# Kernel tuning notes

Hardware: AMD Instinct MI355X
Metric: run time of the kernel (lower is better)

## Reference

```python
import jax, jax.numpy as jnp
import numpy as np

B, S, D, H, DM = 2, 2048, 1024, 16, 4
HD = D // H  # head_dim = 64
EPS = 1e-5


def setup_inputs() -> dict:
    key = jax.random.key(0)
    ks = jax.random.split(key, 8)
    s = 0.02
    return {
        "x": jax.random.normal(ks[0], (B, S, D), jnp.float32),
        "wq": jax.random.normal(ks[1], (D, D), jnp.float32) * s,
        "wk": jax.random.normal(ks[2], (D, D), jnp.float32) * s,
        "wv": jax.random.normal(ks[3], (D, D), jnp.float32) * s,
        "wo": jax.random.normal(ks[4], (D, D), jnp.float32) * s,
        "bo": jnp.zeros((D,), jnp.float32),
        "ln1_scale": jnp.ones((D,), jnp.float32),
        "ln1_shift": jnp.zeros((D,), jnp.float32),
        "ln2_scale": jnp.ones((D,), jnp.float32),
        "ln2_shift": jnp.zeros((D,), jnp.float32),
        "w1": jax.random.normal(ks[5], (DM * D, D), jnp.float32) * s,
        "b1": jnp.zeros((DM * D,), jnp.float32),
        "w2": jax.random.normal(ks[6], (D, DM * D), jnp.float32) * s,
        "b2": jnp.zeros((D,), jnp.float32),
    }


def _layernorm(x, scale, shift):
    mean = jnp.mean(x, axis=-1, keepdims=True)
    var = jnp.var(x, axis=-1, keepdims=True)  # unbiased=False
    return scale * (x - mean) * jax.lax.rsqrt(var + EPS) + shift


def _attn(x, wq, wk, wv, wo, bo):
    b, n, d = x.shape
    # torch Linear: y = x @ W.T
    q = (x @ wq.T).reshape(b, n, H, HD).transpose(0, 2, 1, 3)  # [b,h,n,hd]
    k = (x @ wk.T).reshape(b, n, H, HD).transpose(0, 2, 1, 3)
    v = (x @ wv.T).reshape(b, n, H, HD).transpose(0, 2, 1, 3)
    scores = jnp.einsum("bhqd,bhkd->bhqk", q, k)
    causal = jnp.tril(jnp.ones((n, n), bool))
    scores = jnp.where(causal, scores, -jnp.inf)
    w = jax.nn.softmax(scores / np.sqrt(HD).astype(np.float32), axis=-1)
    ctx = jnp.einsum("bhqk,bhkd->bhqd", w, v)
    ctx = ctx.transpose(0, 2, 1, 3).reshape(b, n, d)
    return ctx @ wo.T + bo


def reference(x, wq, wk, wv, wo, bo, ln1_scale, ln1_shift, ln2_scale, ln2_shift, w1, b1, w2, b2):
    h = x + _attn(_layernorm(x, ln1_scale, ln1_shift), wq, wk, wv, wo, bo)
    y = _layernorm(h, ln2_scale, ln2_shift)
    y = jax.nn.relu(y @ w1.T + b1) @ w2.T + b2
    return h + y
```

## Files before the change

kernel.cpp:

```cpp
#include <hip/hip_runtime.h>
#include <hip/hip_bf16.h>

#define DEV __device__ __forceinline__

typedef __attribute__((ext_vector_type(8))) short bf8;
typedef __attribute__((ext_vector_type(4))) float f4;
typedef __attribute__((ext_vector_type(16))) float f16x;

DEV unsigned short f2bf(float f) {
  union { __hip_bfloat16 h; unsigned short u; } c;
  c.h = __float2bfloat16(f);
  return c.u;
}
DEV unsigned int pk2(float a, float b) {
  union { __hip_bfloat162 h; unsigned int u; } c;
  c.h = __hip_bfloat162(__float2bfloat16(a), __float2bfloat16(b));
  return c.u;
}

DEV int2 swz_tile(int ob, int nxt, int nyt) {
  const int nb = nxt * nyt;
  const int cpx = nb >> 3;
  const int W = (ob & 7) * cpx + (ob >> 3);
  const int scw = 4 * nyt;
  const int sc = W / scw, rem = W - sc * scw;
  return make_int2(rem >> 2, sc * 4 + (rem & 3));
}

template<bool BIAS, bool RELU, bool OUTBF, bool WRVT>
__global__ __launch_bounds__(512, 2) void gemm_bt256(
    const unsigned short* __restrict__ A, const unsigned short* __restrict__ B,
    const float* __restrict__ bias, void* __restrict__ Cout,
    int M, int N, int K, int ldc, unsigned short* __restrict__ vtout, int nyt)
{
  __shared__ unsigned short Sl[2][2][256 * 64];
  const int t = threadIdx.x;
  const int w = t >> 6, l = t & 63;
  const int wr = w >> 2, wc = w & 3;
  int2 tt = swz_tile((int)blockIdx.x, N >> 8, nyt);
  const int m0 = tt.x * 256, n0 = tt.y * 256;

  const int srow = w * 32 + (l >> 3);
  const int scol = 8 * ((l & 7) ^ (l >> 3));
  const unsigned short* Ab = A + (size_t)(m0 + srow) * K + scol;
  const unsigned short* Bb = B + (size_t)(n0 + srow) * K + scol;
  const int sdst = w * 2048 + l * 8;

  auto STAGE = [&](int slot, int kt) {
#pragma unroll
    for (int i = 0; i < 4; ++i) {
      __builtin_amdgcn_global_load_lds(
          (const __attribute__((address_space(1))) void*)(Ab + (size_t)i * 8 * K + kt * 64),
          (__attribute__((address_space(3))) void*)(&Sl[slot][0][sdst + i * 512]), 16, 0, 0);
      __builtin_amdgcn_global_load_lds(
          (const __attribute__((address_space(1))) void*)(Bb + (size_t)i * 8 * K + kt * 64),
          (__attribute__((address_space(3))) void*)(&Sl[slot][1][sdst + i * 512]), 16, 0, 0);
    }
  };

  const f4 fz = {0.f, 0.f, 0.f, 0.f};
  f4 acc[8][4];
#pragma unroll
  for (int i = 0; i < 8; ++i)
#pragma unroll
    for (int j = 0; j < 4; ++j) acc[i][j] = fz;

  const int NT = K >> 6;
  STAGE(0, 0);
  __syncthreads();

  for (int T = 0; T < NT; ++T) {
    if (T + 1 < NT) STAGE((T + 1) & 1, T + 1);
    const int sl = T & 1;
#pragma unroll
    for (int ks = 0; ks < 2; ++ks) {
      const int cb = (ks * 64 + ((l >> 4) * 16)) ^ ((l & 7) << 4);
      bf8 af[8], bg[4];
#pragma unroll
      for (int m = 0; m < 8; ++m)
        af[m] = *(const bf8*)((const char*)&Sl[sl][0][(wr * 128 + m * 16 + (l & 15)) * 64] + cb);
#pragma unroll
      for (int n = 0; n < 4; ++n)
        bg[n] = *(const bf8*)((const char*)&Sl[sl][1][(wc * 64 + n * 16 + (l & 15)) * 64] + cb);
      __builtin_amdgcn_s_setprio(1);
#pragma unroll
      for (int m = 0; m < 8; ++m)
#pragma unroll
        for (int n = 0; n < 4; ++n)
          acc[m][n] = __builtin_amdgcn_mfma_f32_16x16x32_bf16(af[m], bg[n], acc[m][n], 0, 0, 0);
      __builtin_amdgcn_s_setprio(0);
    }
    __syncthreads();
  }

#pragma unroll
  for (int n = 0; n < 4; ++n) {
    const int col = n0 + wc * 64 + n * 16 + (l & 15);
    float bv = 0.f;
    if (BIAS) bv = bias[col];
    const bool isv = WRVT && (col >= 2048);
    const int hh = (col - 2048) >> 6, dd = (col - 2048) & 63;
#pragma unroll
    for (int m = 0; m < 8; ++m) {
#pragma unroll
      for (int r = 0; r < 4; ++r) {
        const int row = m0 + wr * 128 + m * 16 + ((l >> 4) * 4) + r;
        float v = acc[m][n][r] + bv;
        if (RELU) v = fmaxf(v, 0.f);
        if (WRVT && isv) {
          const int bb = row >> 11, ss = row & 2047;
          vtout[((size_t)(bb * 16 + hh) * 64 + dd) * 2048 + ss] = f2bf(v);
        } else if (OUTBF) {
          ((unsigned short*)Cout)[(size_t)row * ldc + col] = f2bf(v);
        } else {
          ((float*)Cout)[(size_t)row * ldc + col] = v;
        }
      }
    }
  }
}

template<bool BIAS, bool RELU, bool RESID, bool OUTBF>
__global__ __launch_bounds__(256) void gemm_bt(
    const unsigned short* __restrict__ A, const unsigned short* __restrict__ B,
    const float* __restrict__ bias, const float* __restrict__ resid,
    void* __restrict__ Cout, int M, int N, int K, int ldc, int nyt)
{
  __shared__ unsigned short Al[2][128 * 32];
  __shared__ unsigned short Bl[2][128 * 32];
  const int t = threadIdx.x;
  const int w = t >> 6, l = t & 63;
  const int wr = w >> 1, wc = w & 1;
  int2 tt = swz_tile((int)blockIdx.x, N >> 7, nyt);
  const int m0 = tt.x * 128, n0 = tt.y * 128;

  const int srow = w * 16 + (l >> 2);
  const int scsw = ((l & 3) * 8) ^ (((srow >> 1) & 3) << 3);
  const unsigned short* Ab = A + (size_t)(m0 + srow) * K + scsw;
  const unsigned short* Bb = B + (size_t)(n0 + srow) * K + scsw;
  const int sdst = w * 512 + l * 8;

  auto STAGE = [&](int slot, int k0) {
#pragma unroll
    for (int i = 0; i < 2; ++i) {
      __builtin_amdgcn_global_load_lds(
          (const __attribute__((address_space(1))) void*)(Ab + (size_t)i * 64 * K + k0),
          (__attribute__((address_space(3))) void*)(&Al[slot][sdst + i * 2048]), 16, 0, 0);
      __builtin_amdgcn_global_load_lds(
          (const __attribute__((address_space(1))) void*)(Bb + (size_t)i * 64 * K + k0),
          (__attribute__((address_space(3))) void*)(&Bl[slot][sdst + i * 2048]), 16, 0, 0);
    }
  };

  const f4 fz = {0.f, 0.f, 0.f, 0.f};
  f4 acc[4][4];
#pragma unroll
  for (int i = 0; i < 4; ++i)
#pragma unroll
    for (int j = 0; j < 4; ++j) acc[i][j] = fz;

  const int NT = K >> 5;
  STAGE(0, 0);
  __syncthreads();

  for (int T = 0; T < NT; ++T) {
    if (T + 1 < NT) STAGE((T + 1) & 1, (T + 1) * 32);
    const int sl = T & 1;
    const int rdcol = ((l >> 4) * 8) ^ ((((l & 15) >> 1) & 3) << 3);
    bf8 af[4], bg[4];
#pragma unroll
    for (int am = 0; am < 4; ++am)
      af[am] = *(const bf8*)&Al[sl][(wr * 64 + am * 16 + (l & 15)) * 32 + rdcol];
#pragma unroll
    for (int bn = 0; bn < 4; ++bn)
      bg[bn] = *(const bf8*)&Bl[sl][(wc * 64 + bn * 16 + (l & 15)) * 32 + rdcol];
    __builtin_amdgcn_s_setprio(1);
#pragma unroll
    for (int am = 0; am < 4; ++am)
#pragma unroll
      for (int bn = 0; bn < 4; ++bn)
        acc[am][bn] = __builtin_amdgcn_mfma_f32_16x16x32_bf16(af[am], bg[bn], acc[am][bn], 0, 0, 0);
    __builtin_amdgcn_s_setprio(0);
    __syncthreads();
  }

#pragma unroll
  for (int bn = 0; bn < 4; ++bn) {
    const int col = n0 + wc * 64 + bn * 16 + (l & 15);
    float bv = 0.f;
    if (BIAS) bv = bias[col];
#pragma unroll
    for (int am = 0; am < 4; ++am) {
#pragma unroll
      for (int r = 0; r < 4; ++r) {
        const int row = m0 + wr * 64 + am * 16 + ((l >> 4) * 4) + r;
        float v = acc[am][bn][r] + bv;
        if (RELU) v = fmaxf(v, 0.f);
        if (RESID) v += resid[(size_t)row * ldc + col];
        if (OUTBF) ((unsigned short*)Cout)[(size_t)row * ldc + col] = f2bf(v);
        else       ((float*)Cout)[(size_t)row * ldc + col] = v;
      }
    }
  }
}

__global__ __launch_bounds__(128, 2) void attn_kernel(
    const unsigned short* __restrict__ qk, const unsigned short* __restrict__ vt,
    unsigned short* __restrict__ ctx)
{
  __shared__ unsigned short Ks[2][64 * 64];
  __shared__ unsigned short Vs[2][64 * 64];

  const int t = threadIdx.x;
  const int w = t >> 6, l = t & 63;
  const int hi = l >> 5, q = l & 31;
  const int j = blockIdx.x;
  const int h = blockIdx.y, b = blockIdx.z;
  const unsigned short* qbase = qk + ((size_t)b * 2048) * 2048 + h * 64;
  const unsigned short* kbase = qbase + 1024;
  const unsigned short* vbase = vt + ((size_t)(b * 16 + h)) * 64 * 2048;

  auto STAGE = [&](int buf, int it) {
#pragma unroll
    for (int s = 0; s < 4; ++s) {
      const int row = s * 16 + (t >> 3);
      const int cb = (t & 7) * 16;
      const int sb = cb ^ ((row & 7) << 4);
      __builtin_amdgcn_global_load_lds(
          (const __attribute__((address_space(1))) void*)
              (kbase + (size_t)(it * 64 + row) * 2048 + (sb >> 1)),
          (__attribute__((address_space(3))) void*)(&Ks[buf][row * 64 + (cb >> 1)]),
          16, 0, 0);
      __builtin_amdgcn_global_load_lds(
          (const __attribute__((address_space(1))) void*)
              (vbase + (size_t)row * 2048 + it * 64 + (sb >> 1)),
          (__attribute__((address_space(3))) void*)(&Vs[buf][row * 64 + (cb >> 1)]),
          16, 0, 0);
    }
  };

  for (int pass = 0; pass < 2; ++pass) {
    const int qtile = pass ? j : 31 - j;
    const int q0w = qtile * 64 + w * 32;
    bf8 qf[4];
#pragma unroll
    for (int ksl = 0; ksl < 4; ++ksl)
      qf[ksl] = *(const bf8*)(qbase + (size_t)(q0w + q) * 2048 + ksl * 16 + hi * 8);

    f16x oacc[2];
#pragma unroll
    for (int dn = 0; dn < 2; ++dn)
#pragma unroll
      for (int i = 0; i < 16; ++i) oacc[dn][i] = 0.f;
    float m_ = -1e30f, l_ = 0.f;

    const int nit = qtile + 1;
    STAGE(0, 0);
    __syncthreads();

    for (int it = 0; it < nit; ++it) {
      const int buf = it & 1;
      if (it + 1 < nit) STAGE(buf ^ 1, it + 1);
      const int kb0 = it * 64;

      f16x s0, s1;
#pragma unroll
      for (int i = 0; i < 16; ++i) { s0[i] = 0.f; s1[i] = 0.f; }
#pragma unroll
      for (int ksl = 0; ksl < 4; ++ksl) {
        const int cbq = ((ksl * 16 + hi * 8) * 2);
        const int r0 = q, r1 = 32 + q;
        bf8 k0 = *(const bf8*)((const char*)&Ks[buf][r0 * 64] + (cbq ^ ((r0 & 7) << 4)));
        bf8 k1 = *(const bf8*)((const char*)&Ks[buf][r1 * 64] + (cbq ^ ((r1 & 7) << 4)));
        s0 = __builtin_amdgcn_mfma_f32_32x32x16_bf16(k0, qf[ksl], s0, 0, 0, 0);
        s1 = __builtin_amdgcn_mfma_f32_32x32x16_bf16(k1, qf[ksl], s1, 0, 0, 0);
      }

      float p[32];
      if (kb0 + 63 > q0w) {
#pragma unroll
        for (int i = 0; i < 16; ++i) {
          const int key = kb0 + (i & 3) + 8 * (i >> 2) + 4 * hi;
          p[i]      = (key <= q0w + q)      ? s0[i] : -1e30f;
          p[16 + i] = (key + 32 <= q0w + q) ? s1[i] : -1e30f;
        }
      } else {
#pragma unroll
        for (int i = 0; i < 16; ++i) { p[i] = s0[i]; p[16 + i] = s1[i]; }
      }

      float tm[16];
#pragma unroll
      for (int i = 0; i < 16; ++i) tm[i] = fmaxf(p[i], p[16 + i]);
#pragma unroll
      for (int st = 8; st >= 1; st >>= 1)
#pragma unroll
        for (int i = 0; i < 8; ++i)
          if (i < st) tm[i] = fmaxf(tm[i], tm[i + st]);
      const float pmax = fmaxf(tm[0], __shfl_xor(tm[0], 32));
      if (__any(pmax > m_ + 8.0f)) {
        const float mn = fmaxf(m_, pmax);
        const float alpha = __expf(m_ - mn);
        m_ = mn;
        l_ *= alpha;
#pragma unroll
        for (int dn = 0; dn < 2; ++dn)
#pragma unroll
          for (int i = 0; i < 16; ++i) oacc[dn][i] *= alpha;
      }
#pragma unroll
      for (int i = 0; i < 32; ++i) p[i] = __expf(p[i] - m_);
      float ts[16];
#pragma unroll
      for (int i = 0; i < 16; ++i) ts[i] = p[i] + p[16 + i];
#pragma unroll
      for (int st = 8; st >= 1; st >>= 1)
#pragma unroll
        for (int i = 0; i < 8; ++i)
          if (i < st) ts[i] += ts[i + st];
      l_ += ts[0] + __shfl_xor(ts[0], 32);

#pragma unroll
      for (int sg = 0; sg < 2; ++sg) {
        const float* pp = p + sg * 16;
        unsigned int wds[8];
#pragma unroll
        for (int m = 0; m < 4; ++m) {
          wds[m * 2]     = pk2(pp[4 * m], pp[4 * m + 1]);
          wds[m * 2 + 1] = pk2(pp[4 * m + 2], pp[4 * m + 3]);
        }
#pragma unroll
        for (int kq = 0; kq < 2; ++kq) {
          unsigned int x0 = __shfl_xor((int)(hi ? wds[4 * kq]     : wds[4 * kq + 2]), 32);
          unsigned int x1 = __shfl_xor((int)(hi ? wds[4 * kq + 1] : wds[4 * kq + 3]), 32);
          union { unsigned int u[4]; bf8 v; } pu;
          pu.u[0] = hi ? x0 : wds[4 * kq];
          pu.u[1] = hi ? x1 : wds[4 * kq + 1];
          pu.u[2] = hi ? wds[4 * kq + 2] : x0;
          pu.u[3] = hi ? wds[4 * kq + 3] : x1;
          const bf8 pf = pu.v;
#pragma unroll
          for (int dn = 0; dn < 2; ++dn) {
            const int row = dn * 32 + q;
            const int cb = ((sg * 32 + kq * 16 + hi * 8) * 2) ^ ((row & 7) << 4);
            bf8 vf = *(const bf8*)((const char*)&Vs[buf][row * 64] + cb);
            oacc[dn] = __builtin_amdgcn_mfma_f32_32x32x16_bf16(vf, pf, oacc[dn], 0, 0, 0);
          }
        }
      }
      __syncthreads();
    }

    const float inv = 1.0f / l_;
    unsigned short* crow = ctx + ((size_t)(b * 2048 + q0w + q)) * 1024 + h * 64;
#pragma unroll
    for (int dn = 0; dn < 2; ++dn)
#pragma unroll
      for (int m = 0; m < 4; ++m) {
        const int d0 = dn * 32 + 8 * m + 4 * hi;
        *(unsigned int*)(crow + d0)     = pk2(oacc[dn][4 * m] * inv, oacc[dn][4 * m + 1] * inv);
        *(unsigned int*)(crow + d0 + 2) = pk2(oacc[dn][4 * m + 2] * inv, oacc[dn][4 * m + 3] * inv);
      }
  }
}

__global__ __launch_bounds__(256) void ln_kernel(
    const float* __restrict__ x, const float* __restrict__ sc,
    const float* __restrict__ sh, unsigned short* __restrict__ out)
{
  const int row = blockIdx.x, t = threadIdx.x;
  float4 v = ((const float4*)x)[(size_t)row * 256 + t];
  float s = v.x + v.y + v.z + v.w;
  float q = v.x * v.x + v.y * v.y + v.z * v.z + v.w * v.w;
#pragma unroll
  for (int off = 1; off < 64; off <<= 1) {
    s += __shfl_xor(s, off);
    q += __shfl_xor(q, off);
  }
  __shared__ float red[8];
  const int w = t >> 6, l = t & 63;
  if (l == 0) { red[w] = s; red[4 + w] = q; }
  __syncthreads();
  s = red[0] + red[1] + red[2] + red[3];
  q = red[4] + red[5] + red[6] + red[7];
  const float mean = s * (1.0f / 1024.0f);
  const float var = q * (1.0f / 1024.0f) - mean * mean;
  const float rstd = rsqrtf(var + 1e-5f);
  float4 scv = ((const float4*)sc)[t];
  float4 shv = ((const float4*)sh)[t];
  uint2 p;
  p.x = pk2(scv.x * (v.x - mean) * rstd + shv.x, scv.y * (v.y - mean) * rstd + shv.y);
  p.y = pk2(scv.z * (v.z - mean) * rstd + shv.z, scv.w * (v.w - mean) * rstd + shv.w);
  ((uint2*)out)[(size_t)row * 256 + t] = p;
}

__global__ __launch_bounds__(256) void cvt_weights(
    const float* __restrict__ wq, const float* __restrict__ wk,
    const float* __restrict__ wv, const float* __restrict__ wo,
    const float* __restrict__ w1, const float* __restrict__ w2,
    unsigned short* __restrict__ dst)
{
  const int M1 = 1 << 20;
  const int n4 = (12 * M1) / 4;
  const int stride = gridDim.x * 256;
  for (int i4 = blockIdx.x * 256 + threadIdx.x; i4 < n4; i4 += stride) {
    const size_t i = (size_t)i4 * 4;
    const int mi = (int)(i >> 20);
    const float* src;
    size_t off;
    float sc = 1.0f;
    if (mi < 4) {
      src = mi == 0 ? wq : mi == 1 ? wk : mi == 2 ? wv : wo;
      off = i & (size_t)(M1 - 1);
      if (mi == 0) sc = 0.125f;
    } else if (mi < 8) {
      src = w1; off = i - (size_t)4 * M1;
    } else {
      src = w2; off = i - (size_t)8 * M1;
    }
    float4 v = *(const float4*)(src + off);
    uint2 pq;
    pq.x = pk2(v.x * sc, v.y * sc);
    pq.y = pk2(v.z * sc, v.w * sc);
    ((uint2*)dst)[i4] = pq;
  }
}

extern "C" void kernel_launch(void* const* d_in, const int* in_sizes, int n_in,
                              void* d_out, int out_size, void* d_ws, size_t ws_size,
                              hipStream_t stream)
{
  const float* x    = (const float*)d_in[0];
  const float* wq   = (const float*)d_in[1];
  const float* wk   = (const float*)d_in[2];
  const float* wv   = (const float*)d_in[3];
  const float* wo   = (const float*)d_in[4];
  const float* bo   = (const float*)d_in[5];
  const float* ln1s = (const float*)d_in[6];
  const float* ln1b = (const float*)d_in[7];
  const float* ln2s = (const float*)d_in[8];
  const float* ln2b = (const float*)d_in[9];
  const float* w1   = (const float*)d_in[10];
  const float* b1   = (const float*)d_in[11];
  const float* w2   = (const float*)d_in[12];
  const float* b2   = (const float*)d_in[13];
  float* out = (float*)d_out;

  const int M = 4096;

  unsigned short* ws   = (unsigned short*)d_ws;
  unsigned short* lnb  = ws;
  unsigned short* qkvw = lnb  + (size_t)4096 * 1024;
  unsigned short* wob  = qkvw + (size_t)3072 * 1024;
  unsigned short* w1b  = wob  + (size_t)1024 * 1024;
  unsigned short* w2b  = w1b  + (size_t)4096 * 1024;
  unsigned short* qkb  = w2b  + (size_t)4096 * 1024;
  unsigned short* vtb  = qkb  + (size_t)4096 * 2048;
  unsigned short* ctxb = vtb  + (size_t)32 * 64 * 2048;
  float* hf = (float*)(ctxb + (size_t)4096 * 1024);

  cvt_weights<<<2048, 256, 0, stream>>>(wq, wk, wv, wo, w1, w2, qkvw);

  ln_kernel<<<M, 256, 0, stream>>>(x, ln1s, ln1b, lnb);
  gemm_bt256<false, false, true, true><<<192, 512, 0, stream>>>(
      lnb, qkvw, nullptr, qkb, M, 3072, 1024, 2048, vtb, 16);
  attn_kernel<<<dim3(16, 16, 2), 128, 0, stream>>>(qkb, vtb, ctxb);
  gemm_bt<true, false, true, false><<<256, 256, 0, stream>>>(
      ctxb, wob, bo, x, hf, M, 1024, 1024, 1024, 32);
  ln_kernel<<<M, 256, 0, stream>>>(hf, ln2s, ln2b, lnb);
  gemm_bt256<true, true, true, false><<<256, 512, 0, stream>>>(
      lnb, w1b, b1, qkb, M, 4096, 1024, 4096, nullptr, 16);
  gemm_bt<true, false, true, false><<<256, 256, 0, stream>>>(
      qkb, w2b, b2, hf, out, M, 1024, 4096, 1024, 32);
}
```

Measured before the change: 272.6 us.

## Rewrite attention to read K/V directly from global, per-wave tiles with XCD mapping

```diff
diff --git a/kernel.cpp b/kernel.cpp
--- a/kernel.cpp
+++ b/kernel.cpp
@@ -204,164 +204,141 @@
   }
 }
 
-__global__ __launch_bounds__(128, 2) void attn_kernel(
+__global__ __launch_bounds__(256) void attn_kernel(
     const unsigned short* __restrict__ qk, const unsigned short* __restrict__ vt,
     unsigned short* __restrict__ ctx)
 {
-  __shared__ unsigned short Ks[2][64 * 64];
-  __shared__ unsigned short Vs[2][64 * 64];
-
   const int t = threadIdx.x;
   const int w = t >> 6, l = t & 63;
   const int hi = l >> 5, q = l & 31;
-  const int j = blockIdx.x;
-  const int h = blockIdx.y, b = blockIdx.z;
+  const int bid = blockIdx.x;
+  const int xcd = bid & 7, j = bid >> 3;
+  const int bh = xcd * 4 + (j >> 4);
+  const int b = bh >> 4, h = bh & 15;
+  const int tile = 63 - ((j & 15) * 4 + w);
+  const int q0w = tile * 32;
+
   const unsigned short* qbase = qk + ((size_t)b * 2048) * 2048 + h * 64;
   const unsigned short* kbase = qbase + 1024;
-  const unsigned short* vbase = vt + ((size_t)(b * 16 + h)) * 64 * 2048;
-
-  auto STAGE = [&](int buf, int it) {
-#pragma unroll
-    for (int s = 0; s < 4; ++s) {
-      const int row = s * 16 + (t >> 3);
-      const int cb = (t & 7) * 16;
-      const int sb = cb ^ ((row & 7) << 4);
-      __builtin_amdgcn_global_load_lds(
-          (const __attribute__((address_space(1))) void*)
-              (kbase + (size_t)(it * 64 + row) * 2048 + (sb >> 1)),
-          (__attribute__((address_space(3))) void*)(&Ks[buf][row * 64 + (cb >> 1)]),
-          16, 0, 0);
-      __builtin_amdgcn_global_load_lds(
-          (const __attribute__((address_space(1))) void*)
-              (vbase + (size_t)row * 2048 + it * 64 + (sb >> 1)),
-          (__attribute__((address_space(3))) void*)(&Vs[buf][row * 64 + (cb >> 1)]),
-          16, 0, 0);
-    }
-  };
-
-  for (int pass = 0; pass < 2; ++pass) {
-    const int qtile = pass ? j : 31 - j;
-    const int q0w = qtile * 64 + w * 32;
-    bf8 qf[4];
-#pragma unroll
-    for (int ksl = 0; ksl < 4; ++ksl)
-      qf[ksl] = *(const bf8*)(qbase + (size_t)(q0w + q) * 2048 + ksl * 16 + hi * 8);
-
-    f16x oacc[2];
-#pragma unroll
-    for (int dn = 0; dn < 2; ++dn)
-#pragma unroll
-      for (int i = 0; i < 16; ++i) oacc[dn][i] = 0.f;
-    float m_ = -1e30f, l_ = 0.f;
-
-    const int nit = qtile + 1;
-    STAGE(0, 0);
-    __syncthreads();
-
-    for (int it = 0; it < nit; ++it) {
-      const int buf = it & 1;
-      if (it + 1 < nit) STAGE(buf ^ 1, it + 1);
-      const int kb0 = it * 64;
-
-      f16x s0, s1;
-#pragma unroll
-      for (int i = 0; i < 16; ++i) { s0[i] = 0.f; s1[i] = 0.f; }
-#pragma unroll
-      for (int ksl = 0; ksl < 4; ++ksl) {
-        const int cbq = ((ksl * 16 + hi * 8) * 2);
-        const int r0 = q, r1 = 32 + q;
-        bf8 k0 = *(const bf8*)((const char*)&Ks[buf][r0 * 64] + (cbq ^ ((r0 & 7) << 4)));
-        bf8 k1 = *(const bf8*)((const char*)&Ks[buf][r1 * 64] + (cbq ^ ((r1 & 7) << 4)));
-        s0 = __builtin_amdgcn_mfma_f32_32x32x16_bf16(k0, qf[ksl], s0, 0, 0, 0);
-        s1 = __builtin_amdgcn_mfma_f32_32x32x16_bf16(k1, qf[ksl], s1, 0, 0, 0);
+  const unsigned short* vbase = vt + (size_t)bh * 64 * 2048;
+
+  const unsigned short* qrow  = qbase + (size_t)(q0w + q) * 2048 + hi * 8;
+  const unsigned short* krow  = kbase + (size_t)q * 2048 + hi * 8;
+  const unsigned short* vrow0 = vbase + (size_t)q * 2048 + hi * 8;
+  const unsigned short* vrow1 = vrow0 + (size_t)32 * 2048;
+
+  bf8 qf[4];
+#pragma unroll
+  for (int ksl = 0; ksl < 4; ++ksl)
+    qf[ksl] = *(const bf8*)(qrow + ksl * 16);
+
+  f16x oacc[2];
+#pragma unroll
+  for (int dn = 0; dn < 2; ++dn)
+#pragma unroll
+    for (int i = 0; i < 16; ++i) oacc[dn][i] = 0.f;
+  float m_ = -1e30f, l_ = 0.f;
+
+  const int nit = (tile >> 1) + 1;
+
+  for (int it = 0; it < nit; ++it) {
+    const int kb0 = it * 64;
+    const unsigned short* kit = krow + (size_t)kb0 * 2048;
+
+    f16x s0, s1;
+#pragma unroll
+    for (int i = 0; i < 16; ++i) { s0[i] = 0.f; s1[i] = 0.f; }
+#pragma unroll
+    for (int ksl = 0; ksl < 4; ++ksl) {
+      bf8 k0 = *(const bf8*)(kit + ksl * 16);
+      bf8 k1 = *(const bf8*)(kit + (size_t)32 * 2048 + ksl * 16);
+      s0 = __builtin_amdgcn_mfma_f32_32x32x16_bf16(k0, qf[ksl], s0, 0, 0, 0);
+      s1 = __builtin_amdgcn_mfma_f32_32x32x16_bf16(k1, qf[ksl], s1, 0, 0, 0);
+    }
+
+    float p[32];
+    if (it == nit - 1) {
+#pragma unroll
+      for (int i = 0; i < 16; ++i) {
+        const int key = kb0 + (i & 3) + 8 * (i >> 2) + 4 * hi;
+        p[i]      = (key <= q0w + q)      ? s0[i] : -1e30f;
+        p[16 + i] = (key + 32 <= q0w + q) ? s1[i] : -1e30f;
       }
-
-      float p[32];
-      if (kb0 + 63 > q0w) {
-#pragma unroll
-        for (int i = 0; i < 16; ++i) {
-          const int key = kb0 + (i & 3) + 8 * (i >> 2) + 4 * hi;
-          p[i]      = (key <= q0w + q)      ? s0[i] : -1e30f;
-          p[16 + i] = (key + 32 <= q0w + q) ? s1[i] : -1e30f;
-        }
-      } else {
-#pragma unroll
-        for (int i = 0; i < 16; ++i) { p[i] = s0[i]; p[16 + i] = s1[i]; }
+    } else {
+#pragma unroll
+      for (int i = 0; i < 16; ++i) { p[i] = s0[i]; p[16 + i] = s1[i]; }
+    }
+
+    float tm[16];
+#pragma unroll
+    for (int i = 0; i < 16; ++i) tm[i] = fmaxf(p[i], p[16 + i]);
+#pragma unroll
+    for (int st = 8; st >= 1; st >>= 1)
+#pragma unroll
+      for (int i = 0; i < 8; ++i)
+        if (i < st) tm[i] = fmaxf(tm[i], tm[i + st]);
+    const float pmax = fmaxf(tm[0], __shfl_xor(tm[0], 32));
+    if (__any(pmax > m_ + 11.54f)) {
+      const float mn = fmaxf(m_, pmax);
+      const float alpha = __builtin_amdgcn_exp2f(m_ - mn);
+      m_ = mn;
+      l_ *= alpha;
+#pragma unroll
+      for (int dn = 0; dn < 2; ++dn)
+#pragma unroll
+        for (int i = 0; i < 16; ++i) oacc[dn][i] *= alpha;
+    }
+#pragma unroll
+    for (int i = 0; i < 32; ++i) p[i] = __builtin_amdgcn_exp2f(p[i] - m_);
+    float ts[16];
+#pragma unroll
+    for (int i = 0; i < 16; ++i) ts[i] = p[i] + p[16 + i];
+#pragma unroll
+    for (int st = 8; st >= 1; st >>= 1)
+#pragma unroll
+      for (int i = 0; i < 8; ++i)
+        if (i < st) ts[i] += ts[i + st];
+    l_ += ts[0] + __shfl_xor(ts[0], 32);
+
+#pragma unroll
+    for (int sg = 0; sg < 2; ++sg) {
+      const float* pp = p + sg * 16;
+      unsigned int wds[8];
+#pragma unroll
+      for (int m = 0; m < 4; ++m) {
+        wds[m * 2]     = pk2(pp[4 * m], pp[4 * m + 1]);
+        wds[m * 2 + 1] = pk2(pp[4 * m + 2], pp[4 * m + 3]);
       }
-
-      float tm[16];
-#pragma unroll
-      for (int i = 0; i < 16; ++i) tm[i] = fmaxf(p[i], p[16 + i]);
-#pragma unroll
-      for (int st = 8; st >= 1; st >>= 1)
-#pragma unroll
-        for (int i = 0; i < 8; ++i)
-          if (i < st) tm[i] = fmaxf(tm[i], tm[i + st]);
-      const float pmax = fmaxf(tm[0], __shfl_xor(tm[0], 32));
-      if (__any(pmax > m_ + 8.0f)) {
-        const float mn = fmaxf(m_, pmax);
-        const float alpha = __expf(m_ - mn);
-        m_ = mn;
-        l_ *= alpha;
-#pragma unroll
-        for (int dn = 0; dn < 2; ++dn)
-#pragma unroll
-          for (int i = 0; i < 16; ++i) oacc[dn][i] *= alpha;
-      }
-#pragma unroll
-      for (int i = 0; i < 32; ++i) p[i] = __expf(p[i] - m_);
-      float ts[16];
-#pragma unroll
-      for (int i = 0; i < 16; ++i) ts[i] = p[i] + p[16 + i];
-#pragma unroll
-      for (int st = 8; st >= 1; st >>= 1)
-#pragma unroll
-        for (int i = 0; i < 8; ++i)
-          if (i < st) ts[i] += ts[i + st];
-      l_ += ts[0] + __shfl_xor(ts[0], 32);
-
-#pragma unroll
-      for (int sg = 0; sg < 2; ++sg) {
-        const float* pp = p + sg * 16;
-        unsigned int wds[8];
-#pragma unroll
-        for (int m = 0; m < 4; ++m) {
-          wds[m * 2]     = pk2(pp[4 * m], pp[4 * m + 1]);
-          wds[m * 2 + 1] = pk2(pp[4 * m + 2], pp[4 * m + 3]);
-        }
-#pragma unroll
-        for (int kq = 0; kq < 2; ++kq) {
-          unsigned int x0 = __shfl_xor((int)(hi ? wds[4 * kq]     : wds[4 * kq + 2]), 32);
-          unsigned int x1 = __shfl_xor((int)(hi ? wds[4 * kq + 1] : wds[4 * kq + 3]), 32);
-          union { unsigned int u[4]; bf8 v; } pu;
-          pu.u[0] = hi ? x0 : wds[4 * kq];
-          pu.u[1] = hi ? x1 : wds[4 * kq + 1];
-          pu.u[2] = hi ? wds[4 * kq + 2] : x0;
-          pu.u[3] = hi ? wds[4 * kq + 3] : x1;
-          const bf8 pf = pu.v;
-#pragma unroll
-          for (int dn = 0; dn < 2; ++dn) {
-            const int row = dn * 32 + q;
-            const int cb = ((sg * 32 + kq * 16 + hi * 8) * 2) ^ ((row & 7) << 4);
-            bf8 vf = *(const bf8*)((const char*)&Vs[buf][row * 64] + cb);
-            oacc[dn] = __builtin_amdgcn_mfma_f32_32x32x16_bf16(vf, pf, oacc[dn], 0, 0, 0);
-          }
+#pragma unroll
+      for (int kq = 0; kq < 2; ++kq) {
+        unsigned int x0 = __shfl_xor((int)(hi ? wds[4 * kq]     : wds[4 * kq + 2]), 32);
+        unsigned int x1 = __shfl_xor((int)(hi ? wds[4 * kq + 1] : wds[4 * kq + 3]), 32);
+        union { unsigned int u[4]; bf8 v; } pu;
+        pu.u[0] = hi ? x0 : wds[4 * kq];
+        pu.u[1] = hi ? x1 : wds[4 * kq + 1];
+        pu.u[2] = hi ? wds[4 * kq + 2] : x0;
+        pu.u[3] = hi ? wds[4 * kq + 3] : x1;
+        const bf8 pf = pu.v;
+#pragma unroll
+        for (int dn = 0; dn < 2; ++dn) {
+          const unsigned short* vp = (dn ? vrow1 : vrow0) + kb0 + sg * 32 + kq * 16;
+          bf8 vf = *(const bf8*)vp;
+          oacc[dn] = __builtin_amdgcn_mfma_f32_32x32x16_bf16(vf, pf, oacc[dn], 0, 0, 0);
         }
       }
-      __syncthreads();
-    }
-
-    const float inv = 1.0f / l_;
-    unsigned short* crow = ctx + ((size_t)(b * 2048 + q0w + q)) * 1024 + h * 64;
-#pragma unroll
-    for (int dn = 0; dn < 2; ++dn)
-#pragma unroll
-      for (int m = 0; m < 4; ++m) {
-        const int d0 = dn * 32 + 8 * m + 4 * hi;
-        *(unsigned int*)(crow + d0)     = pk2(oacc[dn][4 * m] * inv, oacc[dn][4 * m + 1] * inv);
-        *(unsigned int*)(crow + d0 + 2) = pk2(oacc[dn][4 * m + 2] * inv, oacc[dn][4 * m + 3] * inv);
-      }
-  }
+    }
+  }
+
+  const float inv = 1.0f / l_;
+  unsigned short* crow = ctx + ((size_t)(b * 2048 + q0w + q)) * 1024 + h * 64;
+#pragma unroll
+  for (int dn = 0; dn < 2; ++dn)
+#pragma unroll
+    for (int m = 0; m < 4; ++m) {
+      const int d0 = dn * 32 + 8 * m + 4 * hi;
+      *(unsigned int*)(crow + d0)     = pk2(oacc[dn][4 * m] * inv, oacc[dn][4 * m + 1] * inv);
+      *(unsigned int*)(crow + d0 + 2) = pk2(oacc[dn][4 * m + 2] * inv, oacc[dn][4 * m + 3] * inv);
+    }
 }
 
 __global__ __launch_bounds__(256) void ln_kernel(
@@ -412,7 +389,7 @@
     if (mi < 4) {
       src = mi == 0 ? wq : mi == 1 ? wk : mi == 2 ? wv : wo;
       off = i & (size_t)(M1 - 1);
-      if (mi == 0) sc = 0.125f;
+      if (mi == 0) sc = 0.125f * 1.44269504088896f;
     } else if (mi < 8) {
       src = w1; off = i - (size_t)4 * M1;
     } else {
@@ -464,7 +441,7 @@
   ln_kernel<<<M, 256, 0, stream>>>(x, ln1s, ln1b, lnb);
   gemm_bt256<false, false, true, true><<<192, 512, 0, stream>>>(
       lnb, qkvw, nullptr, qkb, M, 3072, 1024, 2048, vtb, 16);
-  attn_kernel<<<dim3(16, 16, 2), 128, 0, stream>>>(qkb, vtb, ctxb);
+  attn_kernel<<<512, 256, 0, stream>>>(qkb, vtb, ctxb);
   gemm_bt<true, false, true, false><<<256, 256, 0, stream>>>(
       ctxb, wob, bo, x, hf, M, 1024, 1024, 1024, 32);
   ln_kernel<<<M, 256, 0, stream>>>(hf, ln2s, ln2b, lnb);
```

Measured after the change: 325.6 us. 1.19x slower.

## Split attention into one 64-query tile per block with XCD-aware grid mapping

Applied to the files above, without the earlier changes.

```diff
diff --git a/kernel.cpp b/kernel.cpp
--- a/kernel.cpp
+++ b/kernel.cpp
@@ -204,7 +204,7 @@
   }
 }
 
-__global__ __launch_bounds__(128, 2) void attn_kernel(
+__global__ __launch_bounds__(128) void attn_kernel(
     const unsigned short* __restrict__ qk, const unsigned short* __restrict__ vt,
     unsigned short* __restrict__ ctx)
 {
@@ -214,11 +214,30 @@
   const int t = threadIdx.x;
   const int w = t >> 6, l = t & 63;
   const int hi = l >> 5, q = l & 31;
-  const int j = blockIdx.x;
-  const int h = blockIdx.y, b = blockIdx.z;
+  const int bid = blockIdx.x;
+  const int xcd = bid & 7, j = bid >> 3;
+  const int bh = xcd * 4 + (j >> 5);
+  const int b = bh >> 4, h = bh & 15;
+  const int u = 31 - (j & 31);
+  const int tile = 2 * u + w;
+  const int q0w = tile * 32;
+  const int nit = u + 1;
+
   const unsigned short* qbase = qk + ((size_t)b * 2048) * 2048 + h * 64;
   const unsigned short* kbase = qbase + 1024;
-  const unsigned short* vbase = vt + ((size_t)(b * 16 + h)) * 64 * 2048;
+  const unsigned short* vbase = vt + (size_t)bh * 64 * 2048;
+
+  bf8 qf[4];
+#pragma unroll
+  for (int ksl = 0; ksl < 4; ++ksl)
+    qf[ksl] = *(const bf8*)(qbase + (size_t)(q0w + q) * 2048 + ksl * 16 + hi * 8);
+
+  f16x oacc[2];
+#pragma unroll
+  for (int dn = 0; dn < 2; ++dn)
+#pragma unroll
+    for (int i = 0; i < 16; ++i) oacc[dn][i] = 0.f;
+  float m_ = -1e30f, l_ = 0.f;
 
   auto STAGE = [&](int buf, int it) {
 #pragma unroll
@@ -239,129 +258,116 @@
     }
   };
 
-  for (int pass = 0; pass < 2; ++pass) {
-    const int qtile = pass ? j : 31 - j;
-    const int q0w = qtile * 64 + w * 32;
-    bf8 qf[4];
-#pragma unroll
-    for (int ksl = 0; ksl < 4; ++ksl)
-      qf[ksl] = *(const bf8*)(qbase + (size_t)(q0w + q) * 2048 + ksl * 16 + hi * 8);
-
-    f16x oacc[2];
-#pragma unroll
-    for (int dn = 0; dn < 2; ++dn)
-#pragma unroll
-      for (int i = 0; i < 16; ++i) oacc[dn][i] = 0.f;
-    float m_ = -1e30f, l_ = 0.f;
-
-    const int nit = qtile + 1;
-    STAGE(0, 0);
+  STAGE(0, 0);
+  __syncthreads();
+
+  for (int it = 0; it < nit; ++it) {
+    const int buf = it & 1;
+    if (it + 1 < nit) STAGE(buf ^ 1, it + 1);
+    const int kb0 = it * 64;
+
+    f16x s0, s1;
+#pragma unroll
+    for (int i = 0; i < 16; ++i) { s0[i] = 0.f; s1[i] = 0.f; }
+    __builtin_amdgcn_s_setprio(1);
+#pragma unroll
+    for (int ksl = 0; ksl < 4; ++ksl) {
+      const int cbq = (ksl * 16 + hi * 8) * 2;
+      const int r0 = q, r1 = 32 + q;
+      bf8 k0 = *(const bf8*)((const char*)&Ks[buf][r0 * 64] + (cbq ^ ((r0 & 7) << 4)));
+      bf8 k1 = *(const bf8*)((const char*)&Ks[buf][r1 * 64] + (cbq ^ ((r1 & 7) << 4)));
+      s0 = __builtin_amdgcn_mfma_f32_32x32x16_bf16(k0, qf[ksl], s0, 0, 0, 0);
+      s1 = __builtin_amdgcn_mfma_f32_32x32x16_bf16(k1, qf[ksl], s1, 0, 0, 0);
+    }
+    __builtin_amdgcn_s_setprio(0);
+
+    float p[32];
+    if (it == nit - 1) {
+#pragma unroll
+      for (int i = 0; i < 16; ++i) {
+        const int key = kb0 + (i & 3) + 8 * (i >> 2) + 4 * hi;
+        p[i]      = (key <= q0w + q)      ? s0[i] : -1e30f;
+        p[16 + i] = (key + 32 <= q0w + q) ? s1[i] : -1e30f;
+      }
+    } else {
+#pragma unroll
+      for (int i = 0; i < 16; ++i) { p[i] = s0[i]; p[16 + i] = s1[i]; }
+    }
+
+    float tm[16];
+#pragma unroll
+    for (int i = 0; i < 16; ++i) tm[i] = fmaxf(p[i], p[16 + i]);
+#pragma unroll
+    for (int st = 8; st >= 1; st >>= 1)
+#pragma unroll
+      for (int i = 0; i < 8; ++i)
+        if (i < st) tm[i] = fmaxf(tm[i], tm[i + st]);
+    const float pmax = fmaxf(tm[0], __shfl_xor(tm[0], 32));
+    if (__any(pmax > m_ + 11.54f)) {
+      const float mn = fmaxf(m_, pmax);
+      const float alpha = __builtin_amdgcn_exp2f(m_ - mn);
+      m_ = mn;
+      l_ *= alpha;
+#pragma unroll
+      for (int dn = 0; dn < 2; ++dn)
+#pragma unroll
+        for (int i = 0; i < 16; ++i) oacc[dn][i] *= alpha;
+    }
+#pragma unroll
+    for (int i = 0; i < 32; ++i) p[i] = __builtin_amdgcn_exp2f(p[i] - m_);
+    float ts[16];
+#pragma unroll
+    for (int i = 0; i < 16; ++i) ts[i] = p[i] + p[16 + i];
+#pragma unroll
+    for (int st = 8; st >= 1; st >>= 1)
+#pragma unroll
+      for (int i = 0; i < 8; ++i)
+        if (i < st) ts[i] += ts[i + st];
+    l_ += ts[0] + __shfl_xor(ts[0], 32);
+
+#pragma unroll
+    for (int sg = 0; sg < 2; ++sg) {
+      const float* pp = p + sg * 16;
+      unsigned int wds[8];
+#pragma unroll
+      for (int m = 0; m < 4; ++m) {
+        wds[m * 2]     = pk2(pp[4 * m], pp[4 * m + 1]);
+        wds[m * 2 + 1] = pk2(pp[4 * m + 2], pp[4 * m + 3]);
+      }
+#pragma unroll
+      for (int kq = 0; kq < 2; ++kq) {
+        unsigned int x0 = __shfl_xor((int)(hi ? wds[4 * kq]     : wds[4 * kq + 2]), 32);
+        unsigned int x1 = __shfl_xor((int)(hi ? wds[4 * kq + 1] : wds[4 * kq + 3]), 32);
+        union { unsigned int u[4]; bf8 v; } pu;
+        pu.u[0] = hi ? x0 : wds[4 * kq];
+        pu.u[1] = hi ? x1 : wds[4 * kq + 1];
+        pu.u[2] = hi ? wds[4 * kq + 2] : x0;
+        pu.u[3] = hi ? wds[4 * kq + 3] : x1;
+        const bf8 pf = pu.v;
+        __builtin_amdgcn_s_setprio(1);
+#pragma unroll
+        for (int dn = 0; dn < 2; ++dn) {
+          const int row = dn * 32 + q;
+          const int cb = ((sg * 32 + kq * 16 + hi * 8) * 2) ^ ((row & 7) << 4);
+          bf8 vf = *(const bf8*)((const char*)&Vs[buf][row * 64] + cb);
+          oacc[dn] = __builtin_amdgcn_mfma_f32_32x32x16_bf16(vf, pf, oacc[dn], 0, 0, 0);
+        }
+        __builtin_amdgcn_s_setprio(0);
+      }
+    }
     __syncthreads();
-
-    for (int it = 0; it < nit; ++it) {
-      const int buf = it & 1;
-      if (it + 1 < nit) STAGE(buf ^ 1, it + 1);
-      const int kb0 = it * 64;
-
-      f16x s0, s1;
-#pragma unroll
-      for (int i = 0; i < 16; ++i) { s0[i] = 0.f; s1[i] = 0.f; }
-#pragma unroll
-      for (int ksl = 0; ksl < 4; ++ksl) {
-        const int cbq = ((ksl * 16 + hi * 8) * 2);
-        const int r0 = q, r1 = 32 + q;
-        bf8 k0 = *(const bf8*)((const char*)&Ks[buf][r0 * 64] + (cbq ^ ((r0 & 7) << 4)));
-        bf8 k1 = *(const bf8*)((const char*)&Ks[buf][r1 * 64] + (cbq ^ ((r1 & 7) << 4)));
-        s0 = __builtin_amdgcn_mfma_f32_32x32x16_bf16(k0, qf[ksl], s0, 0, 0, 0);
-        s1 = __builtin_amdgcn_mfma_f32_32x32x16_bf16(k1, qf[ksl], s1, 0, 0, 0);
-      }
-
-      float p[32];
-      if (kb0 + 63 > q0w) {
-#pragma unroll
-        for (int i = 0; i < 16; ++i) {
-          const int key = kb0 + (i & 3) + 8 * (i >> 2) + 4 * hi;
-          p[i]      = (key <= q0w + q)      ? s0[i] : -1e30f;
-          p[16 + i] = (key + 32 <= q0w + q) ? s1[i] : -1e30f;
-        }
-      } else {
-#pragma unroll
-        for (int i = 0; i < 16; ++i) { p[i] = s0[i]; p[16 + i] = s1[i]; }
-      }
-
-      float tm[16];
-#pragma unroll
-      for (int i = 0; i < 16; ++i) tm[i] = fmaxf(p[i], p[16 + i]);
-#pragma unroll
-      for (int st = 8; st >= 1; st >>= 1)
-#pragma unroll
-        for (int i = 0; i < 8; ++i)
-          if (i < st) tm[i] = fmaxf(tm[i], tm[i + st]);
-      const float pmax = fmaxf(tm[0], __shfl_xor(tm[0], 32));
-      if (__any(pmax > m_ + 8.0f)) {
-        const float mn = fmaxf(m_, pmax);
-        const float alpha = __expf(m_ - mn);
-        m_ = mn;
-        l_ *= alpha;
-#pragma unroll
-        for (int dn = 0; dn < 2; ++dn)
-#pragma unroll
-          for (int i = 0; i < 16; ++i) oacc[dn][i] *= alpha;
-      }
-#pragma unroll
-      for (int i = 0; i < 32; ++i) p[i] = __expf(p[i] - m_);
-      float ts[16];
-#pragma unroll
-      for (int i = 0; i < 16; ++i) ts[i] = p[i] + p[16 + i];
-#pragma unroll
-      for (int st = 8; st >= 1; st >>= 1)
-#pragma unroll
-        for (int i = 0; i < 8; ++i)
-          if (i < st) ts[i] += ts[i + st];
-      l_ += ts[0] + __shfl_xor(ts[0], 32);
-
-#pragma unroll
-      for (int sg = 0; sg < 2; ++sg) {
-        const float* pp = p + sg * 16;
-        unsigned int wds[8];
-#pragma unroll
-        for (int m = 0; m < 4; ++m) {
-          wds[m * 2]     = pk2(pp[4 * m], pp[4 * m + 1]);
-          wds[m * 2 + 1] = pk2(pp[4 * m + 2], pp[4 * m + 3]);
-        }
-#pragma unroll
-        for (int kq = 0; kq < 2; ++kq) {
-          unsigned int x0 = __shfl_xor((int)(hi ? wds[4 * kq]     : wds[4 * kq + 2]), 32);
-          unsigned int x1 = __shfl_xor((int)(hi ? wds[4 * kq + 1] : wds[4 * kq + 3]), 32);
-          union { unsigned int u[4]; bf8 v; } pu;
-          pu.u[0] = hi ? x0 : wds[4 * kq];
-          pu.u[1] = hi ? x1 : wds[4 * kq + 1];
-          pu.u[2] = hi ? wds[4 * kq + 2] : x0;
-          pu.u[3] = hi ? wds[4 * kq + 3] : x1;
-          const bf8 pf = pu.v;
-#pragma unroll
-          for (int dn = 0; dn < 2; ++dn) {
-            const int row = dn * 32 + q;
-            const int cb = ((sg * 32 + kq * 16 + hi * 8) * 2) ^ ((row & 7) << 4);
-            bf8 vf = *(const bf8*)((const char*)&Vs[buf][row * 64] + cb);
-            oacc[dn] = __builtin_amdgcn_mfma_f32_32x32x16_bf16(vf, pf, oacc[dn], 0, 0, 0);
-          }
-        }
-      }
-      __syncthreads();
-    }
-
-    const float inv = 1.0f / l_;
-    unsigned short* crow = ctx + ((size_t)(b * 2048 + q0w + q)) * 1024 + h * 64;
-#pragma unroll
-    for (int dn = 0; dn < 2; ++dn)
-#pragma unroll
-      for (int m = 0; m < 4; ++m) {
-        const int d0 = dn * 32 + 8 * m + 4 * hi;
-        *(unsigned int*)(crow + d0)     = pk2(oacc[dn][4 * m] * inv, oacc[dn][4 * m + 1] * inv);
-        *(unsigned int*)(crow + d0 + 2) = pk2(oacc[dn][4 * m + 2] * inv, oacc[dn][4 * m + 3] * inv);
-      }
-  }
+  }
+
+  const float inv = 1.0f / l_;
+  unsigned short* crow = ctx + ((size_t)(b * 2048 + q0w + q)) * 1024 + h * 64;
+#pragma unroll
+  for (int dn = 0; dn < 2; ++dn)
+#pragma unroll
+    for (int m = 0; m < 4; ++m) {
+      const int d0 = dn * 32 + 8 * m + 4 * hi;
+      *(unsigned int*)(crow + d0)     = pk2(oacc[dn][4 * m] * inv, oacc[dn][4 * m + 1] * inv);
+      *(unsigned int*)(crow + d0 + 2) = pk2(oacc[dn][4 * m + 2] * inv, oacc[dn][4 * m + 3] * inv);
+    }
 }
 
 __global__ __launch_bounds__(256) void ln_kernel(
@@ -412,7 +418,7 @@
     if (mi < 4) {
       src = mi == 0 ? wq : mi == 1 ? wk : mi == 2 ? wv : wo;
       off = i & (size_t)(M1 - 1);
-      if (mi == 0) sc = 0.125f;
+      if (mi == 0) sc = 0.125f * 1.44269504088896f;
     } else if (mi < 8) {
       src = w1; off = i - (size_t)4 * M1;
     } else {
@@ -464,7 +470,7 @@
   ln_kernel<<<M, 256, 0, stream>>>(x, ln1s, ln1b, lnb);
   gemm_bt256<false, false, true, true><<<192, 512, 0, stream>>>(
       lnb, qkvw, nullptr, qkb, M, 3072, 1024, 2048, vtb, 16);
-  attn_kernel<<<dim3(16, 16, 2), 128, 0, stream>>>(qkb, vtb, ctxb);
+  attn_kernel<<<1024, 128, 0, stream>>>(qkb, vtb, ctxb);
   gemm_bt<true, false, true, false><<<256, 256, 0, stream>>>(
       ctxb, wob, bo, x, hf, M, 1024, 1024, 1024, 32);
   ln_kernel<<<M, 256, 0, stream>>>(hf, ln2s, ln2b, lnb);
```

Result: slower. 290.5 us (+6.6%).
